# Optimization experiments

Measured on AMD Instinct MI355X. Metric: run time of the kernel, lower is better.

The kernel has to match this reference:

```python
import jax, jax.numpy as jnp
import numpy as np

B, T, E, H, S = 4, 4096, 1024, 16, 64
D = E // H  # head_dim = 64


def setup_inputs() -> dict:
    key = jax.random.key(0)
    ks = jax.random.split(key, 8)
    sc = 0.02
    return {
        "x": jax.random.normal(ks[0], (B, T, E), jnp.float32),
        "state": jax.random.normal(ks[1], (H, B, S), jnp.float32),
        # stacked per-head params (torch Linear weight layout [out, in])
        "A_w": jax.random.normal(ks[2], (H, S, S), jnp.float32) * sc,
        "A_b": jnp.zeros((H, S), jnp.float32),
        "C_w": jax.random.normal(ks[3], (H, D, S), jnp.float32) * sc,
        "C_b": jnp.zeros((H, D), jnp.float32),
        "sm": jax.random.uniform(ks[4], (H, S, D), jnp.float32),  # torch.rand init
        "Wo": jax.random.normal(ks[5], (E, E), jnp.float32) * sc,
        "bo": jnp.zeros((E,), jnp.float32),
    }


def reference(x, state, A_w, A_b, C_w, C_b, sm, Wo, bo):
    b, t, e = x.shape
    h, s = A_b.shape
    d = e // h
    xh = x.reshape(b, t, h, d)  # [B,T,H,D]
    # A(state): state[i].detach() @ A_w[i].T + A_b[i]  -> [H,B,S]
    a_state = jnp.einsum('hbj,hij->hbi', jax.lax.stop_gradient(state), A_w) + A_b[:, None, :]
    # semiseparable_matrix @ x_head^T, transposed back: [B,T,H,S]
    proj = jnp.einsum('hsd,bthd->bths', sm, xh)
    # broadcast A(state) over the sequence dim (faithful to the original)
    new_state = proj + a_state.transpose(1, 0, 2)[:, None]  # [B,T,H,S]
    # C(new_state): [B,T,H,D]
    out_h = jnp.einsum('bths,hds->bthd', new_state, C_w) + C_b
    # concat heads + output projection
    out = out_h.reshape(b, t, e) @ Wo.T + bo  # [B,T,E]
    new_state_stacked = new_state.transpose(2, 0, 1, 3)  # [H,B,T,S]
    return out, new_state_stacked
```

## Files before the change

### kernel.cpp

```cpp
#include <hip/hip_runtime.h>

#define Bz 4
#define Tz 4096
#define Ez 1024
#define Hz 16
#define Sz 64
#define Dz 64
#define MTz (Bz*Tz)

using f32x4  = __attribute__((ext_vector_type(4))) float;
using short8 = __attribute__((ext_vector_type(8))) short;

__device__ __forceinline__ unsigned f2bf(float f){
  unsigned u = __builtin_bit_cast(unsigned, f);
  u = u + 0x7FFFu + ((u >> 16) & 1u);
  return (u >> 16);
}

#define GLL16(gp, lp) __builtin_amdgcn_global_load_lds( \
    (const __attribute__((address_space(1))) unsigned int*)(gp), \
    (__attribute__((address_space(3))) unsigned int*)(lp), 16, 0, 0)

__global__ __launch_bounds__(256) void k1_pre(const float* __restrict__ state,
                                              const float* __restrict__ A_w,
                                              const float* __restrict__ A_b,
                                              const float* __restrict__ C_w,
                                              const float* __restrict__ C_b,
                                              const float* __restrict__ sm,
                                              float* __restrict__ a_state,
                                              float* __restrict__ Mh,
                                              float* __restrict__ bias_f){
  __shared__ float asl[4][64];
  const int blk = blockIdx.x, tid = threadIdx.x;
  const int h = blk >> 2, q4 = blk & 3;
  {
    const int d = q4*16 + (tid >> 4), dp0 = (tid & 15)*4;
    const float* cw  = C_w + (size_t)(h*64 + d)*64;
    const float* smh = sm + (size_t)h*4096 + dp0;
    float ax=0.f, ay=0.f, az=0.f, aw=0.f;
    #pragma unroll 8
    for (int s = 0; s < 64; ++s){
      float c = cw[s];
      float4 m4 = *(const float4*)&smh[s*64];
      ax += c*m4.x; ay += c*m4.y; az += c*m4.z; aw += c*m4.w;
    }
    *(float4*)&Mh[(size_t)h*4096 + d*64 + dp0] = make_float4(ax,ay,az,aw);
  }
  if (q4 == 0){
    {
      const int b = tid >> 6, s = tid & 63;
      const float* aw = A_w + (size_t)(h*64 + s)*64;
      const float* st = state + (size_t)(h*4 + b)*64;
      float a0=A_b[h*64+s], a1=0.f, a2=0.f, a3=0.f;
      #pragma unroll 4
      for (int j = 0; j < 64; j += 4){
        a0 += aw[j]*st[j]; a1 += aw[j+1]*st[j+1];
        a2 += aw[j+2]*st[j+2]; a3 += aw[j+3]*st[j+3];
      }
      float v = (a0+a1)+(a2+a3);
      a_state[(h*4 + b)*64 + s] = v;
      asl[b][s] = v;
    }
    __syncthreads();
    {
      const int b = tid >> 6, d = tid & 63;
      const float* cw = C_w + (size_t)(h*64 + d)*64;
      float a0=C_b[h*64+d], a1=0.f, a2=0.f, a3=0.f;
      #pragma unroll 4
      for (int s = 0; s < 64; s += 4){
        a0 += cw[s]*asl[b][s]; a1 += cw[s+1]*asl[b][s+1];
        a2 += cw[s+2]*asl[b][s+2]; a3 += cw[s+3]*asl[b][s+3];
      }
      bias_f[b*1024 + h*64 + d] = (a0+a1)+(a2+a3);
    }
  }
}

__global__ __launch_bounds__(256) void kfuse(const float* __restrict__ x,
                                             const float* __restrict__ sm,
                                             const float* __restrict__ a_state,
                                             const float* __restrict__ Wo,
                                             const float* __restrict__ Mh,
                                             const float* __restrict__ bias_f,
                                             const float* __restrict__ bo,
                                             unsigned short* __restrict__ xb,
                                             float* __restrict__ out2,
                                             unsigned short* __restrict__ Wb,
                                             float* __restrict__ constb){
  __shared__ alignas(16) char smem[27648];
  const int gblk = blockIdx.x, tid = threadIdx.x;
  if (gblk < 2048){
    unsigned short* Xs = (unsigned short*)smem;
    unsigned short* Ss = (unsigned short*)(smem + 18432);
    const int lin = gblk;
    const int tb = lin & 31, h = (lin >> 5) & 15, b = lin >> 9;
    const int lane = tid & 63, w = tid >> 6;
    const int l15 = lane & 15, l4 = lane >> 4;

    {
      const float* src = sm + (size_t)h*4096;
      #pragma unroll
      for (int cc = 0; cc < 4; ++cc){
        int c = cc*256 + tid;
        int s = c >> 4, c4 = c & 15;
        float4 v = *(const float4*)&src[s*64 + c4*4];
        uint2 pk = make_uint2(f2bf(v.x) | (f2bf(v.y)<<16), f2bf(v.z) | (f2bf(v.w)<<16));
        *(uint2*)&Ss[s*72 + c4*4] = pk;
      }
    }
    {
      const int row0 = b*Tz + tb*128;
      #pragma unroll
      for (int it = 0; it < 4; ++it){
        int id = it*256 + tid;
        int r = id >> 3, c8 = id & 7;
        const float* px = x + (size_t)(row0 + r)*1024 + h*64 + c8*8;
        float4 v0 = *(const float4*)px, v1 = *(const float4*)(px + 4);
        uint4 pk;
        pk.x = f2bf(v0.x) | (f2bf(v0.y)<<16);
        pk.y = f2bf(v0.z) | (f2bf(v0.w)<<16);
        pk.z = f2bf(v1.x) | (f2bf(v1.y)<<16);
        pk.w = f2bf(v1.z) | (f2bf(v1.w)<<16);
        *(uint4*)&Xs[r*72 + c8*8] = pk;
        *(uint4*)(xb + (size_t)(row0 + r)*1024 + h*64 + c8*8) = pk;
      }
    }
    __syncthreads();

    f32x4 acc[2][4];
    #pragma unroll
    for (int j = 0; j < 4; ++j){
      float4 as4 = *(const float4*)&a_state[(h*4 + b)*64 + j*16 + l4*4];
      f32x4 a0; a0[0]=as4.x; a0[1]=as4.y; a0[2]=as4.z; a0[3]=as4.w;
      acc[0][j] = a0; acc[1][j] = a0;
    }
    #pragma unroll
    for (int kk = 0; kk < 2; ++kk){
      short8 a[2], bb[4];
      #pragma unroll
      for (int i = 0; i < 2; ++i)
        a[i] = *(const short8*)(&Xs[(w*32 + i*16 + l15)*72 + kk*32 + l4*8]);
      #pragma unroll
      for (int j = 0; j < 4; ++j)
        bb[j] = *(const short8*)(&Ss[(j*16 + l15)*72 + kk*32 + l4*8]);
      #pragma unroll
      for (int i = 0; i < 2; ++i)
        #pragma unroll
        for (int j = 0; j < 4; ++j)
          acc[i][j] = __builtin_amdgcn_mfma_f32_16x16x32_bf16(bb[j], a[i], acc[i][j], 0, 0, 0);
    }
    const size_t base = (size_t)h*1048576 + ((size_t)b*4096 + tb*128)*64;
    #pragma unroll
    for (int i = 0; i < 2; ++i)
      #pragma unroll
      for (int j = 0; j < 4; ++j){
        float4 o = make_float4(acc[i][j][0], acc[i][j][1], acc[i][j][2], acc[i][j][3]);
        *(float4*)(out2 + base + (size_t)(w*32 + i*16 + l15)*64 + j*16 + l4*4) = o;
      }
  } else if (gblk < 3072){
    float* Mh_l = (float*)smem;
    const int blk = gblk - 2048;
    const int h = blk >> 6, ec = blk & 63;
    #pragma unroll
    for (int it = 0; it < 4; ++it){
      int c = it*256 + tid;
      *(float4*)&Mh_l[c*4] = *(const float4*)&Mh[(size_t)h*4096 + c*4];
    }
    __syncthreads();
    const int dp = tid & 63, er = tid >> 6;
    #pragma unroll
    for (int ee = 0; ee < 4; ++ee){
      const int e = ec*16 + er*4 + ee;
      const float* wo = Wo + (size_t)e*1024 + h*64;
      float a0=0.f,a1=0.f,a2=0.f,a3=0.f;
      #pragma unroll 4
      for (int d = 0; d < 64; d += 4){
        a0 += wo[d]*Mh_l[d*64+dp];     a1 += wo[d+1]*Mh_l[(d+1)*64+dp];
        a2 += wo[d+2]*Mh_l[(d+2)*64+dp]; a3 += wo[d+3]*Mh_l[(d+3)*64+dp];
      }
      Wb[(size_t)e*1024 + h*64 + dp] = (unsigned short)f2bf((a0+a1)+(a2+a3));
    }
  } else {
    const int idx = (gblk - 3072)*4 + (tid >> 6), lane = tid & 63;
    const int b = idx >> 10, e = idx & 1023;
    const float4* wo = (const float4*)(Wo + (size_t)e*1024);
    const float4* bf = (const float4*)(bias_f + (size_t)b*1024);
    float acc = 0.f;
    #pragma unroll
    for (int i = 0; i < 4; ++i){
      float4 w = wo[i*64 + lane], v = bf[i*64 + lane];
      acc += w.x*v.x + w.y*v.y + w.z*v.z + w.w*v.w;
    }
    acc += __shfl_down(acc, 32); acc += __shfl_down(acc, 16); acc += __shfl_down(acc, 8);
    acc += __shfl_down(acc, 4);  acc += __shfl_down(acc, 2);  acc += __shfl_down(acc, 1);
    if (lane == 0) constb[b*1024 + e] = bo[e] + acc;
  }
}

__global__ __launch_bounds__(512, 2) void k5_gemm(const unsigned short* __restrict__ xb,
                                                  const unsigned short* __restrict__ Wb,
                                                  const float* __restrict__ constb,
                                                  float* __restrict__ out){
  __shared__ alignas(16) unsigned short lds[4][2][8192];
  const int blk = blockIdx.x;
  const int swz = (blk & 7)*32 + (blk >> 3);
  const int bm = (swz >> 2)*256, bn = (swz & 3)*256;
  const int tid = threadIdx.x;
  const int lane = tid & 63, w = tid >> 6;
  const int l15 = lane & 15, l4 = lane >> 4;
  const int wr = w >> 2, wc = w & 3;

  const unsigned short* srcA[2];
  const unsigned short* srcB[2];
  #pragma unroll
  for (int q = 0; q < 2; ++q){
    int L = q*512 + w*64 + lane;
    int b = ((L>>2)&1) ^ ((L>>4)&1);
    int r = (L>>3)*2 + b;
    int g = (L&3) ^ ((((L>>3)&1)<<1) | b);
    srcA[q] = xb + (size_t)(bm + r)*1024 + g*8;
    srcB[q] = Wb + (size_t)(bn + r)*1024 + g*8;
  }
  const int dstoff = w*64*8;
  const int lane_off = ((l15*4 + l4) ^ (l15 & 7))*8;

  #pragma unroll
  for (int t = 0; t < 3; ++t){
    #pragma unroll
    for (int q = 0; q < 2; ++q) GLL16(srcA[q] + t*32, &lds[t][0][q*4096 + dstoff]);
    #pragma unroll
    for (int q = 0; q < 2; ++q) GLL16(srcB[q] + t*32, &lds[t][1][q*4096 + dstoff]);
  }
  asm volatile("s_waitcnt vmcnt(8)" ::: "memory");
  __builtin_amdgcn_s_barrier();
  asm volatile("" ::: "memory");

  f32x4 acc[8][4] = {};

  for (int t = 0; t < 32; ++t){
    const unsigned short* At = &lds[t & 3][0][0];
    const unsigned short* Bt = &lds[t & 3][1][0];
    const int ts = (t + 3) & 3;
    short8 bfr[4], afr[4];
    #pragma unroll
    for (int j = 0; j < 4; ++j)
      bfr[j] = *(const short8*)(Bt + (wc*64 + j*16)*32 + lane_off);
    #pragma unroll
    for (int i = 0; i < 4; ++i)
      afr[i] = *(const short8*)(At + (wr*128 + i*16)*32 + lane_off);
    if (t < 29){
      #pragma unroll
      for (int q = 0; q < 2; ++q) GLL16(srcA[q] + (t+3)*32, &lds[ts][0][q*4096 + dstoff]);
    }
    __builtin_amdgcn_s_setprio(1);
    #pragma unroll
    for (int i = 0; i < 4; ++i)
      #pragma unroll
      for (int j = 0; j < 4; ++j)
        acc[i][j] = __builtin_amdgcn_mfma_f32_16x16x32_bf16(bfr[j], afr[i], acc[i][j], 0, 0, 0);
    __builtin_amdgcn_s_setprio(0);
    #pragma unroll
    for (int i = 0; i < 4; ++i)
      afr[i] = *(const short8*)(At + (wr*128 + (4 + i)*16)*32 + lane_off);
    if (t < 29){
      #pragma unroll
      for (int q = 0; q < 2; ++q) GLL16(srcB[q] + (t+3)*32, &lds[ts][1][q*4096 + dstoff]);
    }
    __builtin_amdgcn_s_setprio(1);
    #pragma unroll
    for (int i = 0; i < 4; ++i)
      #pragma unroll
      for (int j = 0; j < 4; ++j)
        acc[4+i][j] = __builtin_amdgcn_mfma_f32_16x16x32_bf16(bfr[j], afr[i], acc[4+i][j], 0, 0, 0);
    __builtin_amdgcn_s_setprio(0);
    if (t < 29)       asm volatile("s_waitcnt vmcnt(8)" ::: "memory");
    else if (t == 29) asm volatile("s_waitcnt vmcnt(4)" ::: "memory");
    else if (t == 30) asm volatile("s_waitcnt vmcnt(0)" ::: "memory");
    if (t < 31){
      __builtin_amdgcn_s_barrier();
      asm volatile("" ::: "memory");
    }
  }

  const int bb = bm >> 12;
  #pragma unroll
  for (int j = 0; j < 4; ++j){
    int n0 = bn + wc*64 + j*16 + l4*4;
    float4 cv = *(const float4*)&constb[bb*1024 + n0];
    #pragma unroll
    for (int i = 0; i < 8; ++i){
      int trow = bm + wr*128 + i*16 + l15;
      float4 o = make_float4(acc[i][j][0] + cv.x, acc[i][j][1] + cv.y,
                             acc[i][j][2] + cv.z, acc[i][j][3] + cv.w);
      *(float4*)(out + (size_t)trow*1024 + n0) = o;
    }
  }
}

extern "C" void kernel_launch(void* const* d_in, const int* in_sizes, int n_in,
                              void* d_out, int out_size, void* d_ws, size_t ws_size,
                              hipStream_t stream){
  const float* x     = (const float*)d_in[0];
  const float* state = (const float*)d_in[1];
  const float* A_w   = (const float*)d_in[2];
  const float* A_b   = (const float*)d_in[3];
  const float* C_w   = (const float*)d_in[4];
  const float* C_b   = (const float*)d_in[5];
  const float* sm    = (const float*)d_in[6];
  const float* Wo    = (const float*)d_in[7];
  const float* bo    = (const float*)d_in[8];
  float* out  = (float*)d_out;
  float* out2 = out + (size_t)MTz*Ez;

  char* ws = (char*)d_ws;
  float* a_state          = (float*)(ws + 0);
  float* Mh               = (float*)(ws + 16384);
  float* bias_f           = (float*)(ws + 278528);
  float* constb           = (float*)(ws + 294912);
  unsigned short* Wb      = (unsigned short*)(ws + 311296);
  unsigned short* xb      = (unsigned short*)(ws + 2408448);

  k1_pre<<<64, 256, 0, stream>>>(state, A_w, A_b, C_w, C_b, sm, a_state, Mh, bias_f);
  kfuse<<<4096, 256, 0, stream>>>(x, sm, a_state, Wo, Mh, bias_f, bo,
                                  xb, out2, Wb, constb);
  k5_gemm<<<256, 512, 0, stream>>>(xb, Wb, constb, out);
}
```

Baseline: 99.55 us.

## Halve GEMM N-tile to 128 and use triple-buffered LDS pipeline

Shrinks the output GEMM block tile from 256x256 to 256x128, doubling the grid to 512 blocks, and cuts LDS staging from four buffers to three with a prefetch distance of two. The intent is to lower LDS and accumulator-register use so two blocks can be resident per CU, improving latency hiding and load balance. In exchange, each A tile is reloaded for twice as many N tiles and the prefetch depth is shorter.

```diff
diff --git a/kernel.cpp b/kernel.cpp
--- a/kernel.cpp
+++ b/kernel.cpp
@@ -201,91 +201,95 @@
                                                   const unsigned short* __restrict__ Wb,
                                                   const float* __restrict__ constb,
                                                   float* __restrict__ out){
-  __shared__ alignas(16) unsigned short lds[4][2][8192];
+  __shared__ alignas(16) unsigned short ldsA[3][8192];
+  __shared__ alignas(16) unsigned short ldsB[3][4096];
   const int blk = blockIdx.x;
-  const int swz = (blk & 7)*32 + (blk >> 3);
-  const int bm = (swz >> 2)*256, bn = (swz & 3)*256;
+  const int swz = (blk & 7)*64 + (blk >> 3);
+  const int bm = (swz >> 3)*256, bn = (swz & 7)*128;
   const int tid = threadIdx.x;
   const int lane = tid & 63, w = tid >> 6;
   const int l15 = lane & 15, l4 = lane >> 4;
   const int wr = w >> 2, wc = w & 3;
 
   const unsigned short* srcA[2];
-  const unsigned short* srcB[2];
+  const unsigned short* srcB0;
   #pragma unroll
   for (int q = 0; q < 2; ++q){
-    int L = q*512 + w*64 + lane;
+    int L = q*512 + tid;
     int b = ((L>>2)&1) ^ ((L>>4)&1);
     int r = (L>>3)*2 + b;
     int g = (L&3) ^ ((((L>>3)&1)<<1) | b);
     srcA[q] = xb + (size_t)(bm + r)*1024 + g*8;
-    srcB[q] = Wb + (size_t)(bn + r)*1024 + g*8;
-  }
-  const int dstoff = w*64*8;
+  }
+  {
+    int L = tid;
+    int b = ((L>>2)&1) ^ ((L>>4)&1);
+    int r = (L>>3)*2 + b;
+    int g = (L&3) ^ ((((L>>3)&1)<<1) | b);
+    srcB0 = Wb + (size_t)(bn + r)*1024 + g*8;
+  }
+  const int dstoff = tid*8;
   const int lane_off = ((l15*4 + l4) ^ (l15 & 7))*8;
 
   #pragma unroll
   for (int t = 0; t < 3; ++t){
-    #pragma unroll
-    for (int q = 0; q < 2; ++q) GLL16(srcA[q] + t*32, &lds[t][0][q*4096 + dstoff]);
-    #pragma unroll
-    for (int q = 0; q < 2; ++q) GLL16(srcB[q] + t*32, &lds[t][1][q*4096 + dstoff]);
-  }
-  asm volatile("s_waitcnt vmcnt(8)" ::: "memory");
+    GLL16(srcA[0] + t*32, &ldsA[t][dstoff]);
+    GLL16(srcA[1] + t*32, &ldsA[t][4096 + dstoff]);
+    GLL16(srcB0  + t*32, &ldsB[t][dstoff]);
+  }
+  asm volatile("s_waitcnt vmcnt(6)" ::: "memory");
   __builtin_amdgcn_s_barrier();
   asm volatile("" ::: "memory");
 
-  f32x4 acc[8][4] = {};
+  f32x4 acc[8][2] = {};
+  int cur = 0, stg = 2;
 
   for (int t = 0; t < 32; ++t){
-    const unsigned short* At = &lds[t & 3][0][0];
-    const unsigned short* Bt = &lds[t & 3][1][0];
-    const int ts = (t + 3) & 3;
-    short8 bfr[4], afr[4];
-    #pragma unroll
-    for (int j = 0; j < 4; ++j)
-      bfr[j] = *(const short8*)(Bt + (wc*64 + j*16)*32 + lane_off);
+    const unsigned short* At = &ldsA[cur][0];
+    const unsigned short* Bt = &ldsB[cur][0];
+    short8 bfr0, bfr1, afr[4];
+    bfr0 = *(const short8*)(Bt + (wc*32 +  0)*32 + lane_off);
+    bfr1 = *(const short8*)(Bt + (wc*32 + 16)*32 + lane_off);
     #pragma unroll
     for (int i = 0; i < 4; ++i)
       afr[i] = *(const short8*)(At + (wr*128 + i*16)*32 + lane_off);
-    if (t < 29){
-      #pragma unroll
-      for (int q = 0; q < 2; ++q) GLL16(srcA[q] + (t+3)*32, &lds[ts][0][q*4096 + dstoff]);
+    if (t <= 29){
+      GLL16(srcA[0] + (t+2)*32, &ldsA[stg][dstoff]);
+      GLL16(srcA[1] + (t+2)*32, &ldsA[stg][4096 + dstoff]);
     }
     __builtin_amdgcn_s_setprio(1);
     #pragma unroll
-    for (int i = 0; i < 4; ++i)
-      #pragma unroll
-      for (int j = 0; j < 4; ++j)
-        acc[i][j] = __builtin_amdgcn_mfma_f32_16x16x32_bf16(bfr[j], afr[i], acc[i][j], 0, 0, 0);
+    for (int i = 0; i < 4; ++i){
+      acc[i][0] = __builtin_amdgcn_mfma_f32_16x16x32_bf16(bfr0, afr[i], acc[i][0], 0, 0, 0);
+      acc[i][1] = __builtin_amdgcn_mfma_f32_16x16x32_bf16(bfr1, afr[i], acc[i][1], 0, 0, 0);
+    }
     __builtin_amdgcn_s_setprio(0);
     #pragma unroll
     for (int i = 0; i < 4; ++i)
       afr[i] = *(const short8*)(At + (wr*128 + (4 + i)*16)*32 + lane_off);
-    if (t < 29){
-      #pragma unroll
-      for (int q = 0; q < 2; ++q) GLL16(srcB[q] + (t+3)*32, &lds[ts][1][q*4096 + dstoff]);
-    }
+    if (t <= 29)
+      GLL16(srcB0 + (t+2)*32, &ldsB[stg][dstoff]);
     __builtin_amdgcn_s_setprio(1);
     #pragma unroll
-    for (int i = 0; i < 4; ++i)
-      #pragma unroll
-      for (int j = 0; j < 4; ++j)
-        acc[4+i][j] = __builtin_amdgcn_mfma_f32_16x16x32_bf16(bfr[j], afr[i], acc[4+i][j], 0, 0, 0);
+    for (int i = 0; i < 4; ++i){
+      acc[4+i][0] = __builtin_amdgcn_mfma_f32_16x16x32_bf16(bfr0, afr[i], acc[4+i][0], 0, 0, 0);
+      acc[4+i][1] = __builtin_amdgcn_mfma_f32_16x16x32_bf16(bfr1, afr[i], acc[4+i][1], 0, 0, 0);
+    }
     __builtin_amdgcn_s_setprio(0);
-    if (t < 29)       asm volatile("s_waitcnt vmcnt(8)" ::: "memory");
-    else if (t == 29) asm volatile("s_waitcnt vmcnt(4)" ::: "memory");
-    else if (t == 30) asm volatile("s_waitcnt vmcnt(0)" ::: "memory");
+    if (t <= 29)      { asm volatile("s_waitcnt vmcnt(3)" ::: "memory"); }
+    else if (t == 30) { asm volatile("s_waitcnt vmcnt(0)" ::: "memory"); }
     if (t < 31){
       __builtin_amdgcn_s_barrier();
       asm volatile("" ::: "memory");
     }
+    cur = (cur == 2) ? 0 : cur + 1;
+    stg = (stg == 2) ? 0 : stg + 1;
   }
 
   const int bb = bm >> 12;
   #pragma unroll
-  for (int j = 0; j < 4; ++j){
-    int n0 = bn + wc*64 + j*16 + l4*4;
+  for (int j = 0; j < 2; ++j){
+    int n0 = bn + wc*32 + j*16 + l4*4;
     float4 cv = *(const float4*)&constb[bb*1024 + n0];
     #pragma unroll
     for (int i = 0; i < 8; ++i){
@@ -323,5 +327,5 @@
   k1_pre<<<64, 256, 0, stream>>>(state, A_w, A_b, C_w, C_b, sm, a_state, Mh, bias_f);
   kfuse<<<4096, 256, 0, stream>>>(x, sm, a_state, Wo, Mh, bias_f, bo,
                                   xb, out2, Wb, constb);
-  k5_gemm<<<256, 512, 0, stream>>>(xb, Wb, constb, out);
-}
+  k5_gemm<<<512, 512, 0, stream>>>(xb, Wb, constb, out);
+}
```

Result: no change. 97.70 us, median of 2 (-1.9%).
